# Kernel tuning notes

Measured on AMD Instinct MI355X. Metric: run time of the kernel, lower is better.

## Reference

```python
import jax, jax.numpy as jnp
import numpy as np

B, N, D_IN, D_H, D_OUT = 32, 512, 512, 512, 512


def _xavier(key, fan_in, fan_out):
    bound = np.sqrt(6.0 / (fan_in + fan_out))
    return jax.random.uniform(key, (fan_in, fan_out), jnp.float32, -bound, bound)


def setup_inputs() -> dict:
    key = jax.random.key(0)
    ks = jax.random.split(key, 8)
    batch_graph = jax.random.normal(ks[0], (B, N, D_IN), jnp.float32)
    adj = jax.random.uniform(ks[1], (B, N, N), jnp.float32)  # per-graph adjacency blocks
    W0 = _xavier(ks[2], D_IN, D_H)
    b0 = jnp.zeros((D_H,), jnp.float32)
    W1 = _xavier(ks[3], D_H, D_H)
    b1 = jnp.zeros((D_H,), jnp.float32)
    W2 = _xavier(ks[4], D_H, D_OUT)
    b2 = jnp.zeros((D_OUT,), jnp.float32)
    return {"batch_graph": batch_graph, "adj": adj,
            "W0": W0, "b0": b0, "W1": W1, "b1": b1, "W2": W2, "b2": b2}


def _gcn_layer(h, adj, W, b):
    # GraphConvolution: adj @ (h @ W) + b, batched per graph.
    # Equivalent to big_adj @ (big_graph @ W) since big_adj is block-diagonal.
    support = jnp.einsum('bnd,de->bne', h, W)
    return jnp.einsum('bnm,bme->bne', adj, support) + b


def reference(batch_graph, adj, W0, b0, W1, b1, W2, b2):
    # dropout is identity at inference time
    h = jax.nn.relu(_gcn_layer(batch_graph, adj, W0, b0))
    h = jax.nn.relu(_gcn_layer(h, adj, W1, b1))
    h = _gcn_layer(h, adj, W2, b2)  # no activation on final layer
    return h  # [B, N, D_OUT] == torch.stack(big_graph.split(N))
```

## Files before the change

kernel.cpp:

```cpp
#include <hip/hip_runtime.h>
#include <stdint.h>

typedef __bf16 bf16x8 __attribute__((ext_vector_type(8)));
typedef float f32x4 __attribute__((ext_vector_type(4)));
typedef unsigned short u16x4 __attribute__((ext_vector_type(4)));

static __device__ __forceinline__ unsigned short f2bf(float f) {
    union { float f; unsigned u; } v; v.f = f;
    unsigned r = (v.u + 0x7FFFu + ((v.u >> 16) & 1u)) >> 16;
    return (unsigned short)r;
}

__global__ void prep_kernel(const float* __restrict__ X,
                            const float* __restrict__ adj,
                            const float* __restrict__ W0,
                            const float* __restrict__ W1,
                            const float* __restrict__ W2,
                            unsigned short* __restrict__ bufH,
                            unsigned short* __restrict__ adjB,
                            unsigned short* __restrict__ Wt) {
    const int bid = blockIdx.x;
    const int t = threadIdx.x;
    if (bid < 16384) {
        const float* src = (bid < 8192) ? X : adj;
        unsigned short* dst = (bid < 8192) ? bufH : adjB;
        const int q = bid & 8191;
        const int i = (q & 7) * 262144 + (q >> 3) * 256 + t;
        f32x4 v = ((const f32x4*)src)[i];
        u16x4 o;
        o.x = f2bf(v.x); o.y = f2bf(v.y); o.z = f2bf(v.z); o.w = f2bf(v.w);
        ((u16x4*)dst)[i] = o;
    } else {
        const int wb = bid - 16384;
        const int z = wb >> 8;
        const int tile = wb & 255;
        const float* W = (z == 0) ? W0 : (z == 1) ? W1 : W2;
        unsigned short* out = Wt + (size_t)z * (512 * 512);
        __shared__ float tileS[32][33];
        const int bx = (tile & 15) * 32, by = (tile >> 4) * 32;
        const int tx = t & 31, ty = t >> 5;
        #pragma unroll
        for (int r = 0; r < 32; r += 8)
            tileS[ty + r][tx] = W[(size_t)(by + ty + r) * 512 + (bx + tx)];
        __syncthreads();
        #pragma unroll
        for (int r = 0; r < 32; r += 8)
            out[(size_t)(bx + ty + r) * 512 + (by + tx)] = f2bf(tileS[tx][ty + r]);
    }
}

template<int LDA, int LDB, int LDO, bool BIAS, bool RELU, bool ADJ, typename OT>
__global__ __launch_bounds__(256, 2)
void gemm_abT_ct(const unsigned short* __restrict__ A,
                 const unsigned short* __restrict__ B,
                 OT* __restrict__ out, const float* __restrict__ bias,
                 long batchA, long batchB, long batchO) {
    __shared__ char SMEM[65536];
    unsigned short (*As)[8192] = (unsigned short (*)[8192])SMEM;
    unsigned short (*Bs)[8192] = (unsigned short (*)[8192])(SMEM + 32768);

    const int tid  = threadIdx.x;
    const int lane = tid & 63;
    const int wave = tid >> 6;
    const int quad = lane >> 4;
    const int l16  = lane & 15;
    const int wm   = wave & 1;
    const int wn   = wave >> 1;

    const int L = blockIdx.x;
    const int x = L & 7;
    const int j = L >> 3;
    int m0, n0;
    long z;
    if constexpr (ADJ) {
        z = 4 * x + (j >> 4);
        const int t4 = j & 15;
        m0 = (t4 & 3) * 128;
        n0 = (t4 >> 2) * 128;
    } else {
        z = 0;
        m0 = (x * 16 + (j >> 2)) * 128;
        n0 = (j & 3) * 128;
    }
    A   += (size_t)z * batchA;
    B   += (size_t)z * batchB;
    out += (size_t)z * batchO;

    const int trow8 = tid >> 3;
    const int tpos8 = (tid & 7) ^ (trow8 & 7);
    const unsigned short* aG = A + (size_t)(m0 + trow8) * LDA + tpos8 * 8;
    const unsigned short* bG = B + (size_t)(n0 + trow8) * LDB + tpos8 * 8;

    f32x4 acc[4][4];
    #pragma unroll
    for (int i = 0; i < 4; ++i)
        #pragma unroll
        for (int j2 = 0; j2 < 4; ++j2) {
            f32x4 zz = {0.f, 0.f, 0.f, 0.f};
            acc[i][j2] = zz;
        }

#define STAGE(buf, ko)                                                         \
    do {                                                                       \
        char* aL = (char*)(As[buf]) + tid * 16;                                \
        char* bL = (char*)(Bs[buf]) + tid * 16;                                \
        _Pragma("unroll")                                                      \
        for (int r = 0; r < 4; ++r)                                            \
            __builtin_amdgcn_global_load_lds(                                  \
                (__attribute__((address_space(1))) void*)(uintptr_t)(aG + (size_t)(r * 32) * LDA + (ko)), \
                (__attribute__((address_space(3))) void*)(aL + r * 4096), 16, 0, 0); \
        _Pragma("unroll")                                                      \
        for (int r = 0; r < 4; ++r)                                            \
            __builtin_amdgcn_global_load_lds(                                  \
                (__attribute__((address_space(1))) void*)(uintptr_t)(bG + (size_t)(r * 32) * LDB + (ko)), \
                (__attribute__((address_space(3))) void*)(bL + r * 4096), 16, 0, 0); \
    } while (0)

#define COMPUTE(buf)                                                           \
    do {                                                                       \
        _Pragma("unroll")                                                      \
        for (int ks = 0; ks < 2; ++ks) {                                       \
            bf16x8 af[4], bfr[4];                                              \
            _Pragma("unroll")                                                  \
            for (int i = 0; i < 4; ++i) {                                      \
                const int row = wm * 64 + i * 16 + l16;                        \
                const int idx = row * 8 + ((ks * 4 + quad) ^ (row & 7));       \
                af[i] = *(const bf16x8*)((const char*)(As[buf]) + idx * 16);   \
            }                                                                  \
            _Pragma("unroll")                                                  \
            for (int j2 = 0; j2 < 4; ++j2) {                                   \
                const int row = wn * 64 + j2 * 16 + l16;                       \
                const int idx = row * 8 + ((ks * 4 + quad) ^ (row & 7));       \
                bfr[j2] = *(const bf16x8*)((const char*)(Bs[buf]) + idx * 16); \
            }                                                                  \
            _Pragma("unroll")                                                  \
            for (int i = 0; i < 4; ++i)                                        \
                _Pragma("unroll")                                              \
                for (int j2 = 0; j2 < 4; ++j2)                                 \
                    acc[i][j2] = __builtin_amdgcn_mfma_f32_16x16x32_bf16(af[i], bfr[j2], acc[i][j2], 0, 0, 0); \
        }                                                                      \
    } while (0)

    STAGE(0, 0);
    STAGE(1, 64);

    #pragma unroll 1
    for (int kp = 0; kp < 4; ++kp) {
        const int ko = kp * 128;
        asm volatile("s_waitcnt vmcnt(8)" ::: "memory");
        __builtin_amdgcn_s_barrier();
        __builtin_amdgcn_s_setprio(1);
        COMPUTE(0);
        __builtin_amdgcn_s_setprio(0);
        asm volatile("s_waitcnt lgkmcnt(0)" ::: "memory");
        __builtin_amdgcn_sched_barrier(0);
        __builtin_amdgcn_s_barrier();
        if (kp < 3) STAGE(0, ko + 128);
        if (kp < 3) asm volatile("s_waitcnt vmcnt(8)" ::: "memory");
        else        asm volatile("s_waitcnt vmcnt(0)" ::: "memory");
        __builtin_amdgcn_s_barrier();
        __builtin_amdgcn_s_setprio(1);
        COMPUTE(1);
        __builtin_amdgcn_s_setprio(0);
        asm volatile("s_waitcnt lgkmcnt(0)" ::: "memory");
        __builtin_amdgcn_sched_barrier(0);
        __builtin_amdgcn_s_barrier();
        if (kp < 3) STAGE(1, ko + 192);
    }
#undef STAGE
#undef COMPUTE

    if constexpr (sizeof(OT) == 2) {
        unsigned short* T = (unsigned short*)SMEM;
        #pragma unroll
        for (int i = 0; i < 4; ++i) {
            const int mloc = wm * 64 + i * 16 + quad * 4;
            const int mb = m0 + mloc;
            f32x4 bb = {0.f, 0.f, 0.f, 0.f};
            if constexpr (BIAS) bb = *(const f32x4*)(bias + mb);
            const int ch  = mloc >> 3;
            const int sub = (mloc & 7) * 2;
            #pragma unroll
            for (int j2 = 0; j2 < 4; ++j2) {
                const int nloc = wn * 64 + j2 * 16 + l16;
                f32x4 v = acc[i][j2];
                if constexpr (BIAS) v += bb;
                if constexpr (RELU) {
                    v.x = v.x > 0.f ? v.x : 0.f;
                    v.y = v.y > 0.f ? v.y : 0.f;
                    v.z = v.z > 0.f ? v.z : 0.f;
                    v.w = v.w > 0.f ? v.w : 0.f;
                }
                u16x4 o;
                o.x = f2bf(v.x); o.y = f2bf(v.y); o.z = f2bf(v.z); o.w = f2bf(v.w);
                *(u16x4*)((char*)T + nloc * 256 + ((ch ^ (nloc & 7)) << 4) + sub) = o;
            }
        }
        __syncthreads();
        #pragma unroll
        for (int it = 0; it < 8; ++it) {
            const int n  = (tid >> 4) + 16 * it;
            const int cc = tid & 15;
            f32x4 d = *(const f32x4*)((const char*)T + n * 256 + ((cc ^ (n & 7)) << 4));
            *(f32x4*)((unsigned short*)out + (size_t)(n0 + n) * LDO + m0 + cc * 8) = d;
        }
    } else {
        float* T = (float*)SMEM;
        #pragma unroll
        for (int i = 0; i < 4; ++i) {
            const int mloc = wm * 64 + i * 16 + quad * 4;
            const int mb = m0 + mloc;
            f32x4 bb = {0.f, 0.f, 0.f, 0.f};
            if constexpr (BIAS) bb = *(const f32x4*)(bias + mb);
            const int ch = mloc >> 2;
            #pragma unroll
            for (int j2 = 0; j2 < 4; ++j2) {
                const int nloc = wn * 64 + j2 * 16 + l16;
                f32x4 v = acc[i][j2];
                if constexpr (BIAS) v += bb;
                if constexpr (RELU) {
                    v.x = v.x > 0.f ? v.x : 0.f;
                    v.y = v.y > 0.f ? v.y : 0.f;
                    v.z = v.z > 0.f ? v.z : 0.f;
                    v.w = v.w > 0.f ? v.w : 0.f;
                }
                *(f32x4*)((char*)T + nloc * 512 + ((ch ^ (nloc & 7)) << 4)) = v;
            }
        }
        __syncthreads();
        #pragma unroll
        for (int it = 0; it < 16; ++it) {
            const int n  = (tid >> 4) + 16 * (it >> 1);
            const int cc = (tid & 15) + 16 * (it & 1);
            f32x4 d = *(const f32x4*)((const char*)T + n * 512 + ((cc ^ (n & 7)) << 4));
            *(f32x4*)((float*)out + (size_t)(n0 + n) * LDO + m0 + cc * 4) = d;
        }
    }
}

extern "C" void kernel_launch(void* const* d_in, const int* in_sizes, int n_in,
                              void* d_out, int out_size, void* d_ws, size_t ws_size,
                              hipStream_t stream) {
    (void)in_sizes; (void)n_in; (void)out_size; (void)ws_size;
    const float* X   = (const float*)d_in[0];
    const float* adj = (const float*)d_in[1];
    const float* W0  = (const float*)d_in[2];
    const float* b0  = (const float*)d_in[3];
    const float* W1  = (const float*)d_in[4];
    const float* b1  = (const float*)d_in[5];
    const float* W2  = (const float*)d_in[6];
    const float* b2  = (const float*)d_in[7];
    float* out = (float*)d_out;

    char* ws = (char*)d_ws;
    const size_t SZ = 16777216;
    unsigned short* adjB = (unsigned short*)(ws);
    unsigned short* bufH = (unsigned short*)(ws + SZ);
    unsigned short* tmpT = (unsigned short*)(ws + 2 * SZ);
    unsigned short* Wt   = (unsigned short*)(ws + 3 * SZ);
    const unsigned short* W0t = Wt;
    const unsigned short* W1t = Wt + 262144;
    const unsigned short* W2t = Wt + 2 * 262144;

    prep_kernel<<<16384 + 768, 256, 0, stream>>>(X, adj, W0, W1, W2, bufH, adjB, Wt);

    const long BATCH = 512L * 512L;

    gemm_abT_ct<512, 512, 16384, false, false, false, unsigned short>
        <<<512, 256, 0, stream>>>(bufH, W0t, tmpT, nullptr, 0, 0, 0);
    gemm_abT_ct<16384, 512, 512, true, true, true, unsigned short>
        <<<512, 256, 0, stream>>>(tmpT, adjB, bufH, b0, 512, BATCH, BATCH);
    gemm_abT_ct<512, 512, 16384, false, false, false, unsigned short>
        <<<512, 256, 0, stream>>>(bufH, W1t, tmpT, nullptr, 0, 0, 0);
    gemm_abT_ct<16384, 512, 512, true, true, true, unsigned short>
        <<<512, 256, 0, stream>>>(tmpT, adjB, bufH, b1, 512, BATCH, BATCH);
    gemm_abT_ct<512, 512, 16384, false, false, false, unsigned short>
        <<<512, 256, 0, stream>>>(bufH, W2t, tmpT, nullptr, 0, 0, 0);
    gemm_abT_ct<16384, 512, 512, true, false, true, float>
        <<<512, 256, 0, stream>>>(tmpT, adjB, out, b2, 512, BATCH, BATCH);
}
```

Before: 199.7 us.

## Widen GEMM block tile to 128x256 with 512 threads per block

Doubles the N dimension of each GEMM block tile to 256 and runs 8 waves per block, halving the grid to 256 blocks. A-tile loads are now shared across twice as many output columns, which reduces global/LDS traffic per FLOP. The LDS buffers grow to 96KB, the epilogue is split into two halves to fit the fp32 transpose buffer, and the wait counts are adjusted. The larger footprint may cap residency at one block per CU, and 256 blocks only lightly fill 256 CUs, so there is less latency hiding.

Measured after the change: 204.5 us. +2.4%, slower.

```diff
diff --git a/kernel.cpp b/kernel.cpp
--- a/kernel.cpp
+++ b/kernel.cpp
@@ -50,14 +50,12 @@
 }
 
 template<int LDA, int LDB, int LDO, bool BIAS, bool RELU, bool ADJ, typename OT>
-__global__ __launch_bounds__(256, 2)
+__global__ __launch_bounds__(512, 2)
 void gemm_abT_ct(const unsigned short* __restrict__ A,
                  const unsigned short* __restrict__ B,
                  OT* __restrict__ out, const float* __restrict__ bias,
                  long batchA, long batchB, long batchO) {
-    __shared__ char SMEM[65536];
-    unsigned short (*As)[8192] = (unsigned short (*)[8192])SMEM;
-    unsigned short (*Bs)[8192] = (unsigned short (*)[8192])(SMEM + 32768);
+    __shared__ char SMEM[98304];
 
     const int tid  = threadIdx.x;
     const int lane = tid & 63;
@@ -73,14 +71,14 @@
     int m0, n0;
     long z;
     if constexpr (ADJ) {
-        z = 4 * x + (j >> 4);
-        const int t4 = j & 15;
-        m0 = (t4 & 3) * 128;
-        n0 = (t4 >> 2) * 128;
+        z = 4 * x + (j >> 3);
+        const int loc = j & 7;
+        m0 = (loc & 3) * 128;
+        n0 = (loc >> 2) * 256;
     } else {
         z = 0;
-        m0 = (x * 16 + (j >> 2)) * 128;
-        n0 = (j & 3) * 128;
+        m0 = (x * 16 + (j >> 1)) * 128;
+        n0 = (j & 1) * 256;
     }
     A   += (size_t)z * batchA;
     B   += (size_t)z * batchB;
@@ -102,22 +100,24 @@
 
 #define STAGE(buf, ko)                                                         \
     do {                                                                       \
-        char* aL = (char*)(As[buf]) + tid * 16;                                \
-        char* bL = (char*)(Bs[buf]) + tid * 16;                                \
+        char* aL = SMEM + (buf) * 16384 + tid * 16;                            \
+        char* bL = SMEM + 32768 + (buf) * 32768 + tid * 16;                    \
+        _Pragma("unroll")                                                      \
+        for (int r = 0; r < 2; ++r)                                            \
+            __builtin_amdgcn_global_load_lds(                                  \
+                (__attribute__((address_space(1))) void*)(uintptr_t)(aG + (size_t)(r * 64) * LDA + (ko)), \
+                (__attribute__((address_space(3))) void*)(aL + r * 8192), 16, 0, 0); \
         _Pragma("unroll")                                                      \
         for (int r = 0; r < 4; ++r)                                            \
             __builtin_amdgcn_global_load_lds(                                  \
-                (__attribute__((address_space(1))) void*)(uintptr_t)(aG + (size_t)(r * 32) * LDA + (ko)), \
-                (__attribute__((address_space(3))) void*)(aL + r * 4096), 16, 0, 0); \
-        _Pragma("unroll")                                                      \
-        for (int r = 0; r < 4; ++r)                                            \
-            __builtin_amdgcn_global_load_lds(                                  \
-                (__attribute__((address_space(1))) void*)(uintptr_t)(bG + (size_t)(r * 32) * LDB + (ko)), \
-                (__attribute__((address_space(3))) void*)(bL + r * 4096), 16, 0, 0); \
+                (__attribute__((address_space(1))) void*)(uintptr_t)(bG + (size_t)(r * 64) * LDB + (ko)), \
+                (__attribute__((address_space(3))) void*)(bL + r * 8192), 16, 0, 0); \
     } while (0)
 
 #define COMPUTE(buf)                                                           \
     do {                                                                       \
+        const char* Ab = SMEM + (buf) * 16384;                                 \
+        const char* Bb = SMEM + 32768 + (buf) * 32768;                         \
         _Pragma("unroll")                                                      \
         for (int ks = 0; ks < 2; ++ks) {                                       \
             bf16x8 af[4], bfr[4];                                              \
@@ -125,13 +125,13 @@
             for (int i = 0; i < 4; ++i) {                                      \
                 const int row = wm * 64 + i * 16 + l16;                        \
                 const int idx = row * 8 + ((ks * 4 + quad) ^ (row & 7));       \
-                af[i] = *(const bf16x8*)((const char*)(As[buf]) + idx * 16);   \
+                af[i] = *(const bf16x8*)(Ab + idx * 16);                       \
             }                                                                  \
             _Pragma("unroll")                                                  \
             for (int j2 = 0; j2 < 4; ++j2) {                                   \
                 const int row = wn * 64 + j2 * 16 + l16;                       \
                 const int idx = row * 8 + ((ks * 4 + quad) ^ (row & 7));       \
-                bfr[j2] = *(const bf16x8*)((const char*)(Bs[buf]) + idx * 16); \
+                bfr[j2] = *(const bf16x8*)(Bb + idx * 16);                     \
             }                                                                  \
             _Pragma("unroll")                                                  \
             for (int i = 0; i < 4; ++i)                                        \
@@ -147,7 +147,7 @@
     #pragma unroll 1
     for (int kp = 0; kp < 4; ++kp) {
         const int ko = kp * 128;
-        asm volatile("s_waitcnt vmcnt(8)" ::: "memory");
+        asm volatile("s_waitcnt vmcnt(6)" ::: "memory");
         __builtin_amdgcn_s_barrier();
         __builtin_amdgcn_s_setprio(1);
         COMPUTE(0);
@@ -156,7 +156,7 @@
         __builtin_amdgcn_sched_barrier(0);
         __builtin_amdgcn_s_barrier();
         if (kp < 3) STAGE(0, ko + 128);
-        if (kp < 3) asm volatile("s_waitcnt vmcnt(8)" ::: "memory");
+        if (kp < 3) asm volatile("s_waitcnt vmcnt(6)" ::: "memory");
         else        asm volatile("s_waitcnt vmcnt(0)" ::: "memory");
         __builtin_amdgcn_s_barrier();
         __builtin_amdgcn_s_setprio(1);
@@ -199,7 +199,7 @@
         __syncthreads();
         #pragma unroll
         for (int it = 0; it < 8; ++it) {
-            const int n  = (tid >> 4) + 16 * it;
+            const int n  = (tid >> 4) + 32 * it;
             const int cc = tid & 15;
             f32x4 d = *(const f32x4*)((const char*)T + n * 256 + ((cc ^ (n & 7)) << 4));
             *(f32x4*)((unsigned short*)out + (size_t)(n0 + n) * LDO + m0 + cc * 8) = d;
@@ -207,33 +207,39 @@
     } else {
         float* T = (float*)SMEM;
         #pragma unroll
-        for (int i = 0; i < 4; ++i) {
-            const int mloc = wm * 64 + i * 16 + quad * 4;
-            const int mb = m0 + mloc;
-            f32x4 bb = {0.f, 0.f, 0.f, 0.f};
-            if constexpr (BIAS) bb = *(const f32x4*)(bias + mb);
-            const int ch = mloc >> 2;
+        for (int h = 0; h < 2; ++h) {
+            if ((wn >> 1) == h) {
+                #pragma unroll
+                for (int i = 0; i < 4; ++i) {
+                    const int mloc = wm * 64 + i * 16 + quad * 4;
+                    const int mb = m0 + mloc;
+                    f32x4 bb = {0.f, 0.f, 0.f, 0.f};
+                    if constexpr (BIAS) bb = *(const f32x4*)(bias + mb);
+                    const int ch = mloc >> 2;
+                    #pragma unroll
+                    for (int j2 = 0; j2 < 4; ++j2) {
+                        const int nl = wn * 64 + j2 * 16 + l16 - h * 128;
+                        f32x4 v = acc[i][j2];
+                        if constexpr (BIAS) v += bb;
+                        if constexpr (RELU) {
+                            v.x = v.x > 0.f ? v.x : 0.f;
+                            v.y = v.y > 0.f ? v.y : 0.f;
+                            v.z = v.z > 0.f ? v.z : 0.f;
+                            v.w = v.w > 0.f ? v.w : 0.f;
+                        }
+                        *(f32x4*)((char*)T + nl * 512 + ((ch ^ (nl & 7)) << 4)) = v;
+                    }
+                }
+            }
+            __syncthreads();
             #pragma unroll
-            for (int j2 = 0; j2 < 4; ++j2) {
-                const int nloc = wn * 64 + j2 * 16 + l16;
-                f32x4 v = acc[i][j2];
-                if constexpr (BIAS) v += bb;
-                if constexpr (RELU) {
-                    v.x = v.x > 0.f ? v.x : 0.f;
-                    v.y = v.y > 0.f ? v.y : 0.f;
-                    v.z = v.z > 0.f ? v.z : 0.f;
-                    v.w = v.w > 0.f ? v.w : 0.f;
-                }
-                *(f32x4*)((char*)T + nloc * 512 + ((ch ^ (nloc & 7)) << 4)) = v;
+            for (int it = 0; it < 8; ++it) {
+                const int nl = (tid >> 5) + 16 * it;
+                const int cc = tid & 31;
+                f32x4 d = *(const f32x4*)((const char*)T + nl * 512 + ((cc ^ (nl & 7)) << 4));
+                *(f32x4*)((float*)out + (size_t)(n0 + h * 128 + nl) * LDO + m0 + cc * 4) = d;
             }
-        }
-        __syncthreads();
-        #pragma unroll
-        for (int it = 0; it < 16; ++it) {
-            const int n  = (tid >> 4) + 16 * (it >> 1);
-            const int cc = (tid & 15) + 16 * (it & 1);
-            f32x4 d = *(const f32x4*)((const char*)T + n * 512 + ((cc ^ (n & 7)) << 4));
-            *(f32x4*)((float*)out + (size_t)(n0 + n) * LDO + m0 + cc * 4) = d;
+            if (h == 0) __syncthreads();
         }
     }
 }
@@ -267,15 +273,15 @@
     const long BATCH = 512L * 512L;
 
     gemm_abT_ct<512, 512, 16384, false, false, false, unsigned short>
-        <<<512, 256, 0, stream>>>(bufH, W0t, tmpT, nullptr, 0, 0, 0);
+        <<<256, 512, 0, stream>>>(bufH, W0t, tmpT, nullptr, 0, 0, 0);
     gemm_abT_ct<16384, 512, 512, true, true, true, unsigned short>
-        <<<512, 256, 0, stream>>>(tmpT, adjB, bufH, b0, 512, BATCH, BATCH);
+        <<<256, 512, 0, stream>>>(tmpT, adjB, bufH, b0, 512, BATCH, BATCH);
     gemm_abT_ct<512, 512, 16384, false, false, false, unsigned short>
-        <<<512, 256, 0, stream>>>(bufH, W1t, tmpT, nullptr, 0, 0, 0);
+        <<<256, 512, 0, stream>>>(bufH, W1t, tmpT, nullptr, 0, 0, 0);
     gemm_abT_ct<16384, 512, 512, true, true, true, unsigned short>
-        <<<512, 256, 0, stream>>>(tmpT, adjB, bufH, b1, 512, BATCH, BATCH);
+        <<<256, 512, 0, stream>>>(tmpT, adjB, bufH, b1, 512, BATCH, BATCH);
     gemm_abT_ct<512, 512, 16384, false, false, false, unsigned short>
-        <<<512, 256, 0, stream>>>(bufH, W2t, tmpT, nullptr, 0, 0, 0);
+        <<<256, 512, 0, stream>>>(bufH, W2t, tmpT, nullptr, 0, 0, 0);
     gemm_abT_ct<16384, 512, 512, true, false, true, float>
-        <<<512, 256, 0, stream>>>(tmpT, adjB, out, b2, 512, BATCH, BATCH);
-}
+        <<<256, 512, 0, stream>>>(tmpT, adjB, out, b2, 512, BATCH, BATCH);
+}
```
